# Kernel tuning notes

Measured on AMD Instinct MI355X. Metric: run time of the kernel, lower is better.

The kernel has to match this reference:

```python
import jax, jax.numpy as jnp
import numpy as np

D = 1024
H = 8          # MHA fallback num_heads
DH = D // H
DFF = 4096     # mlp_ratio * hidden_size
EPS = 1e-6


def _ln(x, g, b):
    mu = jnp.mean(x, axis=-1, keepdims=True)
    var = jnp.mean((x - mu) ** 2, axis=-1, keepdims=True)
    return (x - mu) * jax.lax.rsqrt(var + EPS) * g + b


def setup_inputs() -> dict:
    key = jax.random.key(0)
    ks = jax.random.split(key, 16)
    s = 0.02
    return {
        "x": jax.random.normal(ks[0], (8, 1024, D), jnp.float32),
        "c": jax.random.normal(ks[1], (8, D), jnp.float32),
        # Mamba-block (attention fallback) params
        "m_ada_w": jax.random.normal(ks[2], (D, 3 * D), jnp.float32) * s,
        "m_ada_b": jnp.zeros((3 * D,), jnp.float32),
        "m_norm_g": jnp.ones((D,), jnp.float32),
        "m_norm_b": jnp.zeros((D,), jnp.float32),
        "in_proj_w": jax.random.normal(ks[3], (3 * D, D), jnp.float32) * s,
        "in_proj_b": jnp.zeros((3 * D,), jnp.float32),
        "out_proj_w": jax.random.normal(ks[4], (D, D), jnp.float32) * s,
        "out_proj_b": jnp.zeros((D,), jnp.float32),
        # FeedForward-block params
        "f_ada_w": jax.random.normal(ks[5], (D, 3 * D), jnp.float32) * s,
        "f_ada_b": jnp.zeros((3 * D,), jnp.float32),
        "f_norm_g": jnp.ones((D,), jnp.float32),
        "f_norm_b": jnp.zeros((D,), jnp.float32),
        "w1": jax.random.normal(ks[6], (D, DFF), jnp.float32) * s,
        "b1": jnp.zeros((DFF,), jnp.float32),
        "w2": jax.random.normal(ks[7], (DFF, D), jnp.float32) * s,
        "b2": jnp.zeros((D,), jnp.float32),
    }


def reference(x, c, m_ada_w, m_ada_b, m_norm_g, m_norm_b, in_proj_w, in_proj_b,
              out_proj_w, out_proj_b, f_ada_w, f_ada_b, f_norm_g, f_norm_b,
              w1, b1, w2, b2):
    B, N, _ = x.shape
    # ---- MambaBlock (MHA fallback), dropout = identity (eval) ----
    mod = jax.nn.silu(c) @ m_ada_w + m_ada_b              # (B, 3D)
    shift, scale, gate = jnp.split(mod, 3, axis=-1)
    h = _ln(x, m_norm_g, m_norm_b)
    h = h * (1.0 + scale[:, None, :]) + shift[:, None, :]
    qkv = h @ in_proj_w.T + in_proj_b                      # (B, N, 3D)
    q, k, v = jnp.split(qkv, 3, axis=-1)
    q = q.reshape(B, N, H, DH)
    k = k.reshape(B, N, H, DH)
    v = v.reshape(B, N, H, DH)
    scores = jnp.einsum("bqhd,bkhd->bhqk", q, k) / np.sqrt(DH).astype(np.float32)
    attn = jax.nn.softmax(scores, axis=-1)
    o = jnp.einsum("bhqk,bkhd->bqhd", attn, v).reshape(B, N, D)
    o = o @ out_proj_w.T + out_proj_b
    x = x + gate[:, None, :] * o
    # ---- FeedForward block ----
    mod2 = jax.nn.silu(c) @ f_ada_w + f_ada_b
    shift2, scale2, gate2 = jnp.split(mod2, 3, axis=-1)
    h = _ln(x, f_norm_g, f_norm_b)
    h = h * (1.0 + scale2[:, None, :]) + shift2[:, None, :]
    h = jax.nn.gelu(h @ w1 + b1, approximate=False) @ w2 + b2
    return x + gate2[:, None, :] * h
```

## Files before the change

kernel.cpp:

```cpp
#include <hip/hip_runtime.h>

typedef __bf16 bf16x8 __attribute__((ext_vector_type(8)));
typedef float f32x4 __attribute__((ext_vector_type(4)));

__device__ __forceinline__ unsigned short f2bf(float f) {
    unsigned int u = __float_as_uint(f);
    unsigned int r = (u + 0x7FFFu + ((u >> 16) & 1u)) >> 16;
    return (unsigned short)r;
}

__device__ __forceinline__ void gload16(const void* g, void* l) {
    __builtin_amdgcn_global_load_lds(
        (const __attribute__((address_space(1))) unsigned int*)g,
        (__attribute__((address_space(3))) unsigned int*)l, 16, 0, 0);
}

__device__ __forceinline__ void barrier_raw() {
    asm volatile("" ::: "memory");
    __builtin_amdgcn_s_barrier();
    asm volatile("" ::: "memory");
}

__device__ __forceinline__ void vmwait0() {
    asm volatile("s_waitcnt vmcnt(0)" ::: "memory");
}

__device__ __forceinline__ float gelu_fast(float u) {
    float z = 1.595769122f * u + 0.071354816f * u * u * u;
    return u / (1.f + __expf(-z));
}

__global__ __launch_bounds__(256) void f2b4(const float* __restrict__ in,
                                            unsigned short* __restrict__ out) {
    size_t i = ((size_t)blockIdx.x * 256 + threadIdx.x) * 4;
    float4 v = *(const float4*)(in + i);
    ushort4 o;
    o.x = f2bf(v.x); o.y = f2bf(v.y); o.z = f2bf(v.z); o.w = f2bf(v.w);
    *(ushort4*)(out + i) = o;
}

__global__ __launch_bounds__(256) void transpose_f2b(const float* __restrict__ in,
                                                     unsigned short* __restrict__ out,
                                                     int R, int C) {
    __shared__ float tile[32][33];
    int r0 = blockIdx.y * 32, c0 = blockIdx.x * 32;
    int tx = threadIdx.x & 31, ty = threadIdx.x >> 5;
#pragma unroll
    for (int i = 0; i < 4; i++) {
        int r = ty + i * 8;
        tile[r][tx] = in[(size_t)(r0 + r) * C + c0 + tx];
    }
    __syncthreads();
#pragma unroll
    for (int i = 0; i < 4; i++) {
        int r = ty + i * 8;
        out[(size_t)(c0 + r) * R + r0 + tx] = f2bf(tile[tx][r]);
    }
}

__global__ __launch_bounds__(256) void transpose_v(const unsigned short* __restrict__ qkv,
                                                   unsigned short* __restrict__ vt) {
    __shared__ unsigned short tile[32][33];
    int head = blockIdx.z;
    int b = head >> 3;
    int n0 = blockIdx.x * 32, d0 = blockIdx.y * 32;
    int tx = threadIdx.x & 31, ty = threadIdx.x >> 5;
    const unsigned short* src = qkv + (size_t)(b * 1024) * 3072 + 2048 + (head & 7) * 128;
#pragma unroll
    for (int i = 0; i < 4; i++) {
        int n = ty + i * 8;
        tile[n][tx] = src[(size_t)(n0 + n) * 3072 + d0 + tx];
    }
    __syncthreads();
#pragma unroll
    for (int i = 0; i < 4; i++) {
        int d = ty + i * 8;
        vt[((size_t)head * 128 + d0 + d) * 1024 + n0 + tx] = tile[tx][d];
    }
}

__global__ __launch_bounds__(256) void ada_mod_part(const float* __restrict__ c,
                                                    const float* __restrict__ W,
                                                    float* __restrict__ partial) {
    __shared__ float sc[8 * 64];
    int kc = blockIdx.y * 64;
    for (int i = threadIdx.x; i < 512; i += 256) {
        int b = i >> 6, k = i & 63;
        float cv = c[b * 1024 + kc + k];
        sc[i] = cv / (1.f + __expf(-cv));
    }
    __syncthreads();
    int j = blockIdx.x * 256 + threadIdx.x;
    float acc[8] = {0, 0, 0, 0, 0, 0, 0, 0};
    for (int k = 0; k < 64; k++) {
        float w = W[(size_t)(kc + k) * 3072 + j];
#pragma unroll
        for (int b = 0; b < 8; b++) acc[b] += sc[b * 64 + k] * w;
    }
#pragma unroll
    for (int b = 0; b < 8; b++) partial[((size_t)blockIdx.y * 8 + b) * 3072 + j] = acc[b];
}

__global__ __launch_bounds__(256) void ada_reduce(const float* __restrict__ partial,
                                                  const float* __restrict__ bias,
                                                  float* __restrict__ out) {
    int idx = blockIdx.x * 256 + threadIdx.x;
    int b = idx / 3072;
    int jj = idx - b * 3072;
    float s = bias[jj];
#pragma unroll
    for (int ch = 0; ch < 16; ch++) s += partial[((size_t)ch * 8 + b) * 3072 + jj];
    out[idx] = s;
}

__global__ __launch_bounds__(256) void ln_mod_kernel(const float* __restrict__ x,
                                                     const float* __restrict__ gamma,
                                                     const float* __restrict__ beta,
                                                     const float* __restrict__ mods,
                                                     unsigned short* __restrict__ out) {
    int row = blockIdx.x;
    int b = row >> 10;
    float4 v = ((const float4*)(x + (size_t)row * 1024))[threadIdx.x];
    float s = v.x + v.y + v.z + v.w;
    float s2 = v.x * v.x + v.y * v.y + v.z * v.z + v.w * v.w;
#pragma unroll
    for (int d = 1; d < 64; d <<= 1) { s += __shfl_xor(s, d); s2 += __shfl_xor(s2, d); }
    __shared__ float red[8];
    int lane = threadIdx.x & 63, wid = threadIdx.x >> 6;
    if (lane == 0) { red[wid] = s; red[4 + wid] = s2; }
    __syncthreads();
    float S = red[0] + red[1] + red[2] + red[3];
    float S2 = red[4] + red[5] + red[6] + red[7];
    float mu = S * (1.f / 1024.f);
    float var = S2 * (1.f / 1024.f) - mu * mu;
    float rs = rsqrtf(var + 1e-6f);
    const float* mrow = mods + b * 3072;
    int j0 = threadIdx.x * 4;
    float hv[4] = {v.x, v.y, v.z, v.w};
    ushort4 o;
    unsigned short* op = (unsigned short*)&o;
#pragma unroll
    for (int i = 0; i < 4; i++) {
        int j = j0 + i;
        float hh = (hv[i] - mu) * rs * gamma[j] + beta[j];
        hh = hh * (1.f + mrow[1024 + j]) + mrow[j];
        op[i] = f2bf(hh);
    }
    *(ushort4*)(out + (size_t)row * 1024 + j0) = o;
}

template <int NF, int WR, int WC, int EP>
__global__ __launch_bounds__(512) void gemmk(const unsigned short* __restrict__ A,
                                             const unsigned short* __restrict__ Bt,
                                             int N, int K, int nx,
                                             const float* __restrict__ bias,
                                             const float* __restrict__ xres,
                                             const float* __restrict__ mods,
                                             float* __restrict__ outf,
                                             unsigned short* __restrict__ outb) {
    constexpr int BROWS = NF * 64;
    constexpr int MR = 256 / (16 * WR);
    constexpr int NR = BROWS / (16 * WC);
    constexpr int AE = 256 * 32;
    constexpr int BE = BROWS * 32;
    extern __shared__ __align__(16) char smem[];
    __bf16* As = (__bf16*)smem;
    __bf16* Bs = As + 2 * AE;

    int tid = threadIdx.x, lane = tid & 63, wid = tid >> 6;
    int wr = wid / WC, wc = wid % WC;
    int t = lane & 15, g = lane >> 4;

    int nwg = gridDim.x, chunk = nwg >> 3;
    int swz = (blockIdx.x & 7) * chunk + (blockIdx.x >> 3);
    int bx = swz % nx, by = swz / nx;
    int rowA0 = by * 256, colB0 = bx * BROWS;

    int rin = tid >> 2, cq = (tid & 3) * 8;

    auto stage = [&](int nb, int kt1) {
        int k0 = kt1 << 5;
        gload16(A + (size_t)(rowA0 + rin) * K + k0 + cq, (void*)(As + nb * AE + tid * 8));
        gload16(A + (size_t)(rowA0 + 128 + rin) * K + k0 + cq,
                (void*)(As + nb * AE + 4096 + tid * 8));
        gload16(Bt + (size_t)(colB0 + rin) * K + k0 + cq, (void*)(Bs + nb * BE + tid * 8));
        if constexpr (NF == 4)
            gload16(Bt + (size_t)(colB0 + 128 + rin) * K + k0 + cq,
                    (void*)(Bs + nb * BE + 4096 + tid * 8));
    };

    f32x4 acc[MR][NR];
#pragma unroll
    for (int m = 0; m < MR; m++)
#pragma unroll
        for (int n = 0; n < NR; n++) acc[m][n] = (f32x4){0.f, 0.f, 0.f, 0.f};

    stage(0, 0);
    vmwait0();
    barrier_raw();

    int NT = K >> 5;
#pragma unroll 1
    for (int kt = 0; kt < NT; ++kt) {
        const __bf16* Ac = As + (kt & 1) * AE;
        const __bf16* Bc = Bs + (kt & 1) * BE;
        bool more = (kt + 1) < NT;
        if (more) stage((kt & 1) ^ 1, kt + 1);

        bf16x8 a[MR], b[NR];
#pragma unroll
        for (int m = 0; m < MR; m++)
            a[m] = *(const bf16x8*)&Ac[(wr * (MR * 16) + m * 16 + t) * 32 + g * 8];
#pragma unroll
        for (int n = 0; n < NR; n++)
            b[n] = *(const bf16x8*)&Bc[(wc * (NR * 16) + n * 16 + t) * 32 + g * 8];

        __builtin_amdgcn_s_setprio(1);
#pragma unroll
        for (int m = 0; m < MR; m++)
#pragma unroll
            for (int n = 0; n < NR; n++)
                acc[m][n] = __builtin_amdgcn_mfma_f32_16x16x32_bf16(a[m], b[n], acc[m][n], 0, 0, 0);
        __builtin_amdgcn_s_setprio(0);

        if (more) {
            vmwait0();
            barrier_raw();
        }
    }

    int row0 = rowA0 + wr * (MR * 16), col0 = colB0 + wc * (NR * 16);
#pragma unroll
    for (int m = 0; m < MR; m++)
#pragma unroll
        for (int n = 0; n < NR; n++) {
            int col = col0 + n * 16 + t;
#pragma unroll
            for (int r = 0; r < 4; r++) {
                int row = row0 + m * 16 + g * 4 + r;
                float v = acc[m][n][r];
                if (EP == 0) {
                    outb[(size_t)row * N + col] = f2bf(v + bias[col]);
                } else if (EP == 1) {
                    int bb = row >> 10;
                    float gt = mods[bb * 3072 + 2048 + col];
                    outf[(size_t)row * 1024 + col] =
                        xres[(size_t)row * 1024 + col] + gt * (v + bias[col]);
                } else if (EP == 2) {
                    outb[(size_t)row * N + col] = f2bf(gelu_fast(v + bias[col]));
                } else {
                    int bb = row >> 10;
                    float gt = mods[bb * 3072 + 2048 + col];
                    outf[(size_t)row * 1024 + col] += gt * (v + bias[col]);
                }
            }
        }
}

__global__ __launch_bounds__(512, 4) void attn_kernel(const unsigned short* __restrict__ qkv,
                                                      const unsigned short* __restrict__ vt,
                                                      unsigned short* __restrict__ o) {
    extern __shared__ __align__(16) char asmem[];
    __bf16* Ks = (__bf16*)asmem;
    __bf16* Vts = Ks + 2 * 64 * 128;

    int bid = blockIdx.x;
    int logical = (bid & 7) * 64 + (bid >> 3);
    int q0 = (logical & 7) * 128;
    int bh = logical >> 3;
    int b = bh >> 3, h = bh & 7;
    int tid = threadIdx.x, lane = tid & 63, w = tid >> 6;
    int t = lane & 15, g = lane >> 4;
    int swzt = (t & 7) << 4;

    const unsigned short* qbase = qkv + (size_t)(b * 1024) * 3072 + h * 128;
    int qrow = q0 + w * 16 + t;
    bf16x8 qf[4];
#pragma unroll
    for (int ks = 0; ks < 4; ks++)
        qf[ks] = *(const bf16x8*)(qbase + (size_t)qrow * 3072 + ks * 32 + g * 8);

    f32x4 Oa[8];
#pragma unroll
    for (int n = 0; n < 8; n++) Oa[n] = (f32x4){0.f, 0.f, 0.f, 0.f};
    float m_r = -1e30f, l_r = 0.f;
    const float scale = 0.08838834764831845f;

    int krow = tid >> 4;
    int ksrc = (((tid & 15) * 16) ^ ((krow & 7) << 4)) >> 1;
    int vrow = tid >> 3;
    int vsrc = (((tid & 7) * 16) ^ ((vrow & 7) << 4)) >> 1;
    const unsigned short* vtg = vt + (size_t)bh * 128 * 1024;

    auto stage = [&](int buf, int kv0) {
        const unsigned short* kb = qkv + (size_t)(b * 1024 + kv0) * 3072 + 1024 + h * 128;
#pragma unroll
        for (int cc = 0; cc < 2; cc++) {
            gload16(kb + (size_t)(cc * 32 + krow) * 3072 + ksrc,
                    (void*)(Ks + buf * 8192 + cc * 4096 + tid * 8));
            gload16(vtg + (size_t)(cc * 64 + vrow) * 1024 + kv0 + vsrc,
                    (void*)(Vts + buf * 8192 + cc * 4096 + tid * 8));
        }
    };

    stage(0, 0);
    vmwait0();
    barrier_raw();

#pragma unroll 1
    for (int tile = 0; tile < 16; ++tile) {
        int cur = tile & 1;
        bool more = tile < 15;
        if (more) stage(cur ^ 1, (tile + 1) * 64);
        const __bf16* Kc = Ks + cur * 8192;
        const __bf16* Vc = Vts + cur * 8192;

        f32x4 St[4];
#pragma unroll
        for (int n = 0; n < 4; n++) St[n] = (f32x4){0.f, 0.f, 0.f, 0.f};
        __builtin_amdgcn_s_setprio(1);
#pragma unroll
        for (int ks = 0; ks < 4; ks++) {
#pragma unroll
            for (int n = 0; n < 4; n++) {
                bf16x8 kf = *(const bf16x8*)&Kc[(n * 16 + t) * 128 + (((ks * 64 + g * 16) ^ swzt) >> 1)];
                St[n] = __builtin_amdgcn_mfma_f32_16x16x32_bf16(kf, qf[ks], St[n], 0, 0, 0);
            }
        }
        __builtin_amdgcn_s_setprio(0);

        float mx = -1e30f;
#pragma unroll
        for (int n = 0; n < 4; n++)
#pragma unroll
            for (int r = 0; r < 4; r++) mx = fmaxf(mx, St[n][r]);
        mx *= scale;
        mx = fmaxf(mx, __shfl_xor(mx, 16));
        mx = fmaxf(mx, __shfl_xor(mx, 32));
        float mn = fmaxf(m_r, mx);
        float alpha = __expf(m_r - mn);
        m_r = mn;
        float p[4][4];
        float rs = 0.f;
#pragma unroll
        for (int n = 0; n < 4; n++)
#pragma unroll
            for (int r = 0; r < 4; r++) {
                float pv = __expf(St[n][r] * scale - mn);
                p[n][r] = pv;
                rs += pv;
            }
        rs += __shfl_xor(rs, 16);
        rs += __shfl_xor(rs, 32);
        l_r = l_r * alpha + rs;

        unsigned P01[4], P23[4];
#pragma unroll
        for (int n = 0; n < 4; n++) {
            P01[n] = (unsigned)f2bf(p[n][0]) | ((unsigned)f2bf(p[n][1]) << 16);
            P23[n] = (unsigned)f2bf(p[n][2]) | ((unsigned)f2bf(p[n][3]) << 16);
        }

#pragma unroll
        for (int r = 0; r < 4; r++) {
            float ar = __shfl(alpha, (lane & 48) + g * 4 + r);
#pragma unroll
            for (int n2 = 0; n2 < 8; n2++) Oa[n2][r] *= ar;
        }

#pragma unroll
        for (int ks2 = 0; ks2 < 2; ks2++) {
            int e = ks2 * 2, od = ks2 * 2 + 1;
            unsigned s16a = (g < 2) ? P01[e] : P01[od];
            unsigned s16b = (g < 2) ? P23[e] : P23[od];
            unsigned s32a = (g & 1) ? P01[e] : P01[od];
            unsigned s32b = (g & 1) ? P23[e] : P23[od];
            unsigned s48a = (g >= 2) ? P01[e] : P01[od];
            unsigned s48b = (g >= 2) ? P23[e] : P23[od];
            unsigned r16a = __shfl_xor(s16a, 16), r16b = __shfl_xor(s16b, 16);
            unsigned r32a = __shfl_xor(s32a, 32), r32b = __shfl_xor(s32b, 32);
            unsigned r48a = __shfl_xor(s48a, 48), r48b = __shfl_xor(s48b, 48);
            union { unsigned u[4]; bf16x8 v; } pa;
            pa.u[0] = (g == 0) ? P01[e] : (g == 1) ? r48a : (g == 2) ? r32a : r16a;
            pa.u[1] = (g == 0) ? P23[e] : (g == 1) ? r48b : (g == 2) ? r32b : r16b;
            pa.u[2] = (g == 0) ? r16a : (g == 1) ? r32a : (g == 2) ? r48a : P01[od];
            pa.u[3] = (g == 0) ? r16b : (g == 1) ? r32b : (g == 2) ? r48b : P23[od];
            __builtin_amdgcn_s_setprio(1);
#pragma unroll
            for (int n2 = 0; n2 < 8; n2++) {
                bf16x8 vf = *(const bf16x8*)&Vc[(n2 * 16 + t) * 64 + (((ks2 * 64 + g * 16) ^ swzt) >> 1)];
                Oa[n2] = __builtin_amdgcn_mfma_f32_16x16x32_bf16(pa.v, vf, Oa[n2], 0, 0, 0);
            }
            __builtin_amdgcn_s_setprio(0);
        }

        if (more) { vmwait0(); barrier_raw(); }
    }

#pragma unroll
    for (int r = 0; r < 4; r++) {
        float lq = __shfl(l_r, (lane & 48) + g * 4 + r);
        float inv = 1.f / lq;
        int orow = q0 + w * 16 + g * 4 + r;
#pragma unroll
        for (int n2 = 0; n2 < 8; n2++)
            o[(size_t)(b * 1024 + orow) * 1024 + h * 128 + n2 * 16 + t] = f2bf(Oa[n2][r] * inv);
    }
}

extern "C" void kernel_launch(void* const* d_in, const int* in_sizes, int n_in,
                              void* d_out, int out_size, void* d_ws, size_t ws_size,
                              hipStream_t stream) {
    const float* x          = (const float*)d_in[0];
    const float* c          = (const float*)d_in[1];
    const float* m_ada_w    = (const float*)d_in[2];
    const float* m_ada_b    = (const float*)d_in[3];
    const float* m_norm_g   = (const float*)d_in[4];
    const float* m_norm_b   = (const float*)d_in[5];
    const float* in_proj_w  = (const float*)d_in[6];
    const float* in_proj_b  = (const float*)d_in[7];
    const float* out_proj_w = (const float*)d_in[8];
    const float* out_proj_b = (const float*)d_in[9];
    const float* f_ada_w    = (const float*)d_in[10];
    const float* f_ada_b    = (const float*)d_in[11];
    const float* f_norm_g   = (const float*)d_in[12];
    const float* f_norm_b   = (const float*)d_in[13];
    const float* w1         = (const float*)d_in[14];
    const float* b1         = (const float*)d_in[15];
    const float* w2         = (const float*)d_in[16];
    const float* b2         = (const float*)d_in[17];
    float* out = (float*)d_out;
    char* ws = (char*)d_ws;

    unsigned short* Wq   = (unsigned short*)(ws + 0);
    unsigned short* Wo   = (unsigned short*)(ws + 6291456);
    unsigned short* vt   = (unsigned short*)(ws + 8388608);
    unsigned short* W1t  = (unsigned short*)(ws + 8388608);
    unsigned short* W2t  = (unsigned short*)(ws + 16777216);
    float*          modm = (float*)(ws + 25165824);
    float*          modf = (float*)(ws + 25264128);
    unsigned short* hbuf = (unsigned short*)(ws + 25362432);
    float*          part = (float*)(ws + 25362432);
    float*          part2= (float*)(ws + 25362432 + 2097152);
    unsigned short* qkv  = (unsigned short*)(ws + 42139648);
    unsigned short* obuf = (unsigned short*)(ws + 92471296);
    unsigned short* h2   = (unsigned short*)(ws + 42139648);

    hipFuncSetAttribute((const void*)&gemmk<4, 2, 4, 0>, hipFuncAttributeMaxDynamicSharedMemorySize, 65536);
    hipFuncSetAttribute((const void*)&gemmk<4, 2, 4, 2>, hipFuncAttributeMaxDynamicSharedMemorySize, 65536);
    hipFuncSetAttribute((const void*)&gemmk<2, 4, 2, 1>, hipFuncAttributeMaxDynamicSharedMemorySize, 49152);
    hipFuncSetAttribute((const void*)&gemmk<2, 4, 2, 3>, hipFuncAttributeMaxDynamicSharedMemorySize, 49152);
    hipFuncSetAttribute((const void*)&attn_kernel, hipFuncAttributeMaxDynamicSharedMemorySize, 65536);

    hipLaunchKernelGGL(ada_mod_part, dim3(12, 16), dim3(256), 0, stream, c, m_ada_w, part);
    hipLaunchKernelGGL(ada_mod_part, dim3(12, 16), dim3(256), 0, stream, c, f_ada_w, part2);
    hipLaunchKernelGGL(ada_reduce, dim3(96), dim3(256), 0, stream, part, m_ada_b, modm);
    hipLaunchKernelGGL(ada_reduce, dim3(96), dim3(256), 0, stream, part2, f_ada_b, modf);

    hipLaunchKernelGGL(f2b4, dim3(3072), dim3(256), 0, stream, in_proj_w, Wq);
    hipLaunchKernelGGL(f2b4, dim3(1024), dim3(256), 0, stream, out_proj_w, Wo);

    hipLaunchKernelGGL(ln_mod_kernel, dim3(8192), dim3(256), 0, stream, x, m_norm_g, m_norm_b, modm, hbuf);
    hipLaunchKernelGGL(HIP_KERNEL_NAME(gemmk<4, 2, 4, 0>), dim3(384), dim3(512), 65536, stream,
                       hbuf, Wq, 3072, 1024, 12, in_proj_b, (const float*)nullptr,
                       (const float*)nullptr, (float*)nullptr, qkv);
    hipLaunchKernelGGL(transpose_v, dim3(32, 4, 64), dim3(256), 0, stream, qkv, vt);
    hipLaunchKernelGGL(attn_kernel, dim3(512), dim3(512), 65536, stream, qkv, vt, obuf);
    hipLaunchKernelGGL(HIP_KERNEL_NAME(gemmk<2, 4, 2, 1>), dim3(256), dim3(512), 49152, stream,
                       obuf, Wo, 1024, 1024, 8, out_proj_b, x, modm, out, (unsigned short*)nullptr);

    hipLaunchKernelGGL(transpose_f2b, dim3(128, 32), dim3(256), 0, stream, w1, W1t, 1024, 4096);
    hipLaunchKernelGGL(transpose_f2b, dim3(32, 128), dim3(256), 0, stream, w2, W2t, 4096, 1024);

    hipLaunchKernelGGL(ln_mod_kernel, dim3(8192), dim3(256), 0, stream, out, f_norm_g, f_norm_b, modf, hbuf);
    hipLaunchKernelGGL(HIP_KERNEL_NAME(gemmk<4, 2, 4, 2>), dim3(512), dim3(512), 65536, stream,
                       hbuf, W1t, 4096, 1024, 16, b1, (const float*)nullptr,
                       (const float*)nullptr, (float*)nullptr, h2);
    hipLaunchKernelGGL(HIP_KERNEL_NAME(gemmk<2, 4, 2, 3>), dim3(256), dim3(512), 49152, stream,
                       h2, W2t, 1024, 4096, 8, b2, (const float*)nullptr, modf, out,
                       (unsigned short*)nullptr);
}
```

Measured before the change: 404.3 us.

## Replace GEMM kernel with 128x256 tile, BK=64, swizzled LDS and XCD-aware mapping

Replaces the templated GEMM with a single 128x256 tile design. It uses a K-step of 64 with XOR-swizzled LDS staging to avoid bank conflicts, launch bounds of 2 blocks per CU, and explicit XCD-aware block-to-tile mappings (two variants). Halving the barrier count per K and spreading tiles across XCDs for L2 locality should raise MFMA utilisation. The cost is more LDS per block (96 KB), which limits occupancy, and smaller M tiles that reload B more often.

```diff
diff --git a/kernel.cpp b/kernel.cpp
--- a/kernel.cpp
+++ b/kernel.cpp
@@ -149,57 +149,58 @@
     *(ushort4*)(out + (size_t)row * 1024 + j0) = o;
 }
 
-template <int NF, int WR, int WC, int EP>
-__global__ __launch_bounds__(512) void gemmk(const unsigned short* __restrict__ A,
-                                             const unsigned short* __restrict__ Bt,
-                                             int N, int K, int nx,
-                                             const float* __restrict__ bias,
-                                             const float* __restrict__ xres,
-                                             const float* __restrict__ mods,
-                                             float* __restrict__ outf,
-                                             unsigned short* __restrict__ outb) {
-    constexpr int BROWS = NF * 64;
-    constexpr int MR = 256 / (16 * WR);
-    constexpr int NR = BROWS / (16 * WC);
-    constexpr int AE = 256 * 32;
-    constexpr int BE = BROWS * 32;
+template <int CMAP, int EP>
+__global__ __launch_bounds__(512, 2) void gemmv2(const unsigned short* __restrict__ A,
+                                                 const unsigned short* __restrict__ Bt,
+                                                 int N, int K,
+                                                 const float* __restrict__ bias,
+                                                 const float* __restrict__ xres,
+                                                 const float* __restrict__ mods,
+                                                 float* __restrict__ outf,
+                                                 unsigned short* __restrict__ outb) {
+    constexpr int AE = 128 * 64;
+    constexpr int BE = 256 * 64;
     extern __shared__ __align__(16) char smem[];
     __bf16* As = (__bf16*)smem;
     __bf16* Bs = As + 2 * AE;
 
     int tid = threadIdx.x, lane = tid & 63, wid = tid >> 6;
-    int wr = wid / WC, wc = wid % WC;
+    int wr = wid >> 2, wc = wid & 3;
     int t = lane & 15, g = lane >> 4;
-
-    int nwg = gridDim.x, chunk = nwg >> 3;
-    int swz = (blockIdx.x & 7) * chunk + (blockIdx.x >> 3);
-    int bx = swz % nx, by = swz / nx;
-    int rowA0 = by * 256, colB0 = bx * BROWS;
-
-    int rin = tid >> 2, cq = (tid & 3) * 8;
-
-    auto stage = [&](int nb, int kt1) {
-        int k0 = kt1 << 5;
-        gload16(A + (size_t)(rowA0 + rin) * K + k0 + cq, (void*)(As + nb * AE + tid * 8));
-        gload16(A + (size_t)(rowA0 + 128 + rin) * K + k0 + cq,
-                (void*)(As + nb * AE + 4096 + tid * 8));
-        gload16(Bt + (size_t)(colB0 + rin) * K + k0 + cq, (void*)(Bs + nb * BE + tid * 8));
-        if constexpr (NF == 4)
-            gload16(Bt + (size_t)(colB0 + 128 + rin) * K + k0 + cq,
-                    (void*)(Bs + nb * BE + 4096 + tid * 8));
+    int xk = (t & 7) * 8;
+
+    int xcd = blockIdx.x & 7, s = blockIdx.x >> 3;
+    int by, bx;
+    if (CMAP == 0) { by = xcd + 8 * (s & 7); bx = s >> 3; }
+    else           { bx = xcd & 3; by = (xcd >> 2) * 32 + s; }
+    int rowA0 = by * 128, colB0 = bx * 256;
+
+    int rin = tid >> 3, cblk = tid & 7;
+    int scol = (cblk ^ (rin & 7)) * 8;
+
+    auto stage = [&](int nb, int kt) {
+        int k0 = kt << 6;
+#pragma unroll
+        for (int sl = 0; sl < 2; sl++)
+            gload16(A + (size_t)(rowA0 + sl * 64 + rin) * K + k0 + scol,
+                    As + nb * AE + sl * 4096 + tid * 8);
+#pragma unroll
+        for (int sl = 0; sl < 4; sl++)
+            gload16(Bt + (size_t)(colB0 + sl * 64 + rin) * K + k0 + scol,
+                    Bs + nb * BE + sl * 4096 + tid * 8);
     };
 
-    f32x4 acc[MR][NR];
-#pragma unroll
-    for (int m = 0; m < MR; m++)
-#pragma unroll
-        for (int n = 0; n < NR; n++) acc[m][n] = (f32x4){0.f, 0.f, 0.f, 0.f};
+    f32x4 acc[4][4];
+#pragma unroll
+    for (int m = 0; m < 4; m++)
+#pragma unroll
+        for (int n = 0; n < 4; n++) acc[m][n] = (f32x4){0.f, 0.f, 0.f, 0.f};
 
     stage(0, 0);
     vmwait0();
     barrier_raw();
 
-    int NT = K >> 5;
+    int NT = K >> 6;
 #pragma unroll 1
     for (int kt = 0; kt < NT; ++kt) {
         const __bf16* Ac = As + (kt & 1) * AE;
@@ -207,21 +208,23 @@
         bool more = (kt + 1) < NT;
         if (more) stage((kt & 1) ^ 1, kt + 1);
 
-        bf16x8 a[MR], b[NR];
-#pragma unroll
-        for (int m = 0; m < MR; m++)
-            a[m] = *(const bf16x8*)&Ac[(wr * (MR * 16) + m * 16 + t) * 32 + g * 8];
-#pragma unroll
-        for (int n = 0; n < NR; n++)
-            b[n] = *(const bf16x8*)&Bc[(wc * (NR * 16) + n * 16 + t) * 32 + g * 8];
-
-        __builtin_amdgcn_s_setprio(1);
-#pragma unroll
-        for (int m = 0; m < MR; m++)
-#pragma unroll
-            for (int n = 0; n < NR; n++)
-                acc[m][n] = __builtin_amdgcn_mfma_f32_16x16x32_bf16(a[m], b[n], acc[m][n], 0, 0, 0);
-        __builtin_amdgcn_s_setprio(0);
+#pragma unroll
+        for (int ks = 0; ks < 2; ks++) {
+            bf16x8 a[4], b[4];
+#pragma unroll
+            for (int m = 0; m < 4; m++)
+                a[m] = *(const bf16x8*)&Ac[(wr * 64 + m * 16 + t) * 64 + ((ks * 32 + g * 8) ^ xk)];
+#pragma unroll
+            for (int n = 0; n < 4; n++)
+                b[n] = *(const bf16x8*)&Bc[(wc * 64 + n * 16 + t) * 64 + ((ks * 32 + g * 8) ^ xk)];
+            __builtin_amdgcn_s_setprio(1);
+#pragma unroll
+            for (int m = 0; m < 4; m++)
+#pragma unroll
+                for (int n = 0; n < 4; n++)
+                    acc[m][n] = __builtin_amdgcn_mfma_f32_16x16x32_bf16(a[m], b[n], acc[m][n], 0, 0, 0);
+            __builtin_amdgcn_s_setprio(0);
+        }
 
         if (more) {
             vmwait0();
@@ -229,11 +232,11 @@
         }
     }
 
-    int row0 = rowA0 + wr * (MR * 16), col0 = colB0 + wc * (NR * 16);
-#pragma unroll
-    for (int m = 0; m < MR; m++)
-#pragma unroll
-        for (int n = 0; n < NR; n++) {
+    int row0 = rowA0 + wr * 64, col0 = colB0 + wc * 64;
+#pragma unroll
+    for (int m = 0; m < 4; m++)
+#pragma unroll
+        for (int n = 0; n < 4; n++) {
             int col = col0 + n * 16 + t;
 #pragma unroll
             for (int r = 0; r < 4; r++) {
@@ -394,7 +397,10 @@
             __builtin_amdgcn_s_setprio(0);
         }
 
-        if (more) { vmwait0(); barrier_raw(); }
+        if (more) {
+            vmwait0();
+            barrier_raw();
+        }
     }
 
 #pragma unroll
@@ -446,10 +452,10 @@
     unsigned short* obuf = (unsigned short*)(ws + 92471296);
     unsigned short* h2   = (unsigned short*)(ws + 42139648);
 
-    hipFuncSetAttribute((const void*)&gemmk<4, 2, 4, 0>, hipFuncAttributeMaxDynamicSharedMemorySize, 65536);
-    hipFuncSetAttribute((const void*)&gemmk<4, 2, 4, 2>, hipFuncAttributeMaxDynamicSharedMemorySize, 65536);
-    hipFuncSetAttribute((const void*)&gemmk<2, 4, 2, 1>, hipFuncAttributeMaxDynamicSharedMemorySize, 49152);
-    hipFuncSetAttribute((const void*)&gemmk<2, 4, 2, 3>, hipFuncAttributeMaxDynamicSharedMemorySize, 49152);
+    hipFuncSetAttribute((const void*)&gemmv2<0, 0>, hipFuncAttributeMaxDynamicSharedMemorySize, 98304);
+    hipFuncSetAttribute((const void*)&gemmv2<0, 2>, hipFuncAttributeMaxDynamicSharedMemorySize, 98304);
+    hipFuncSetAttribute((const void*)&gemmv2<0, 1>, hipFuncAttributeMaxDynamicSharedMemorySize, 98304);
+    hipFuncSetAttribute((const void*)&gemmv2<1, 3>, hipFuncAttributeMaxDynamicSharedMemorySize, 98304);
     hipFuncSetAttribute((const void*)&attn_kernel, hipFuncAttributeMaxDynamicSharedMemorySize, 65536);
 
     hipLaunchKernelGGL(ada_mod_part, dim3(12, 16), dim3(256), 0, stream, c, m_ada_w, part);
@@ -461,22 +467,22 @@
     hipLaunchKernelGGL(f2b4, dim3(1024), dim3(256), 0, stream, out_proj_w, Wo);
 
     hipLaunchKernelGGL(ln_mod_kernel, dim3(8192), dim3(256), 0, stream, x, m_norm_g, m_norm_b, modm, hbuf);
-    hipLaunchKernelGGL(HIP_KERNEL_NAME(gemmk<4, 2, 4, 0>), dim3(384), dim3(512), 65536, stream,
-                       hbuf, Wq, 3072, 1024, 12, in_proj_b, (const float*)nullptr,
+    hipLaunchKernelGGL(HIP_KERNEL_NAME(gemmv2<0, 0>), dim3(768), dim3(512), 98304, stream,
+                       hbuf, Wq, 3072, 1024, in_proj_b, (const float*)nullptr,
                        (const float*)nullptr, (float*)nullptr, qkv);
     hipLaunchKernelGGL(transpose_v, dim3(32, 4, 64), dim3(256), 0, stream, qkv, vt);
     hipLaunchKernelGGL(attn_kernel, dim3(512), dim3(512), 65536, stream, qkv, vt, obuf);
-    hipLaunchKernelGGL(HIP_KERNEL_NAME(gemmk<2, 4, 2, 1>), dim3(256), dim3(512), 49152, stream,
-                       obuf, Wo, 1024, 1024, 8, out_proj_b, x, modm, out, (unsigned short*)nullptr);
+    hipLaunchKernelGGL(HIP_KERNEL_NAME(gemmv2<0, 1>), dim3(256), dim3(512), 98304, stream,
+                       obuf, Wo, 1024, 1024, out_proj_b, x, modm, out, (unsigned short*)nullptr);
 
     hipLaunchKernelGGL(transpose_f2b, dim3(128, 32), dim3(256), 0, stream, w1, W1t, 1024, 4096);
     hipLaunchKernelGGL(transpose_f2b, dim3(32, 128), dim3(256), 0, stream, w2, W2t, 4096, 1024);
 
     hipLaunchKernelGGL(ln_mod_kernel, dim3(8192), dim3(256), 0, stream, out, f_norm_g, f_norm_b, modf, hbuf);
-    hipLaunchKernelGGL(HIP_KERNEL_NAME(gemmk<4, 2, 4, 2>), dim3(512), dim3(512), 65536, stream,
-                       hbuf, W1t, 4096, 1024, 16, b1, (const float*)nullptr,
+    hipLaunchKernelGGL(HIP_KERNEL_NAME(gemmv2<0, 2>), dim3(1024), dim3(512), 98304, stream,
+                       hbuf, W1t, 4096, 1024, b1, (const float*)nullptr,
                        (const float*)nullptr, (float*)nullptr, h2);
-    hipLaunchKernelGGL(HIP_KERNEL_NAME(gemmk<2, 4, 2, 3>), dim3(256), dim3(512), 49152, stream,
-                       h2, W2t, 1024, 4096, 8, b2, (const float*)nullptr, modf, out,
+    hipLaunchKernelGGL(HIP_KERNEL_NAME(gemmv2<1, 3>), dim3(256), dim3(512), 98304, stream,
+                       h2, W2t, 1024, 4096, b2, (const float*)nullptr, modf, out,
                        (unsigned short*)nullptr);
 }
```

After: 386.8 us. 4.3% less time.
